# Kernel optimization log

Hardware: AMD Instinct MI355X
Metric: run time of the kernel (lower is better)

## Reference

```python
import jax, jax.numpy as jnp
import numpy as np


def setup_inputs() -> dict:
    key = jax.random.key(0)
    ks = jax.random.split(key, 5)
    B, T, D, L = 4, 8192, 1024, 128
    X = jax.random.normal(ks[0], (B, T, D), dtype=jnp.float32)
    attention_mask = jnp.ones((B, T), dtype=jnp.float32)
    sd_dl = 1.0 / np.sqrt(D)  # lecun_normal fan_in = D
    Wk = jax.random.normal(ks[1], (D, L), dtype=jnp.float32) * sd_dl
    Wq = jax.random.normal(ks[2], (D, L), dtype=jnp.float32) * sd_dl
    Wv = jax.random.normal(ks[3], (D, D), dtype=jnp.float32) * sd_dl
    o_proj = jax.random.normal(ks[4], (D, D), dtype=jnp.float32) * sd_dl
    return {"X": X, "attention_mask": attention_mask, "Wk": Wk, "Wq": Wq,
            "Wv": Wv, "o_proj": o_proj, "n_heads": 16}


def reference(X, attention_mask, Wk, Wq, Wv, o_proj, n_heads):
    B, T, D = X.shape
    H = n_heads
    # Projections, laid out time-major as in the original: (T, B, H, *)
    V = jnp.einsum('DM,BTD->TBM', Wv, X).reshape(T, B, H, -1)   # (T,B,H,d)
    Q = jnp.einsum('DL,BTD->TBL', Wq, X).reshape(T, B, H, -1)   # (T,B,H,l)
    K = jnp.einsum('DL,BTD->TBL', Wk, X).reshape(T, B, H, -1)   # (T,B,H,l)
    m = attention_mask.T[:, :, None, None]                       # (T,B,1,1)
    V = V * m
    Qs = jax.nn.softmax(Q, axis=-1)
    maxi = jnp.max(K, axis=0, keepdims=True)                     # global max over T
    K = jnp.exp(K - maxi) * m
    Kv = jnp.einsum('tbhl,tbhd->bhld', K, V)                     # global KV state
    Ksum = K.sum(axis=0)                                         # (B,H,l)
    Kv = Kv / Ksum[..., None]
    y = jnp.einsum('tbhl,bhld->bthd', Qs, Kv).reshape(B, T, D)
    return y @ o_proj
```

## Files before the change

kernel.cpp:

```cpp
#include <hip/hip_runtime.h>
#include <hip/hip_bf16.h>

typedef unsigned short u16;
typedef unsigned int   u32;

typedef __attribute__((ext_vector_type(8))) short short8;
typedef __attribute__((ext_vector_type(4))) float f32x4;

typedef const __attribute__((address_space(1))) void g_void;
typedef __attribute__((address_space(3))) void l_void;

__device__ __forceinline__ float bf2f(u16 u) {
    u32 x = ((u32)u) << 16;
    return __builtin_bit_cast(float, x);
}
__device__ __forceinline__ u16 f2bf(float f) {
    u32 u = __builtin_bit_cast(u32, f);
    u32 r = (u + 0x7FFFu + ((u >> 16) & 1u)) >> 16;
    return (u16)r;
}
__device__ __forceinline__ u32 pack2(float a, float b) {
    return (u32)f2bf(a) | ((u32)f2bf(b) << 16);
}

__global__ void detect_kernel(const u16* __restrict__ X, int* __restrict__ flags) {
    __shared__ int cnt[256];
    int c = 0;
    for (int i = threadIdx.x; i < 16384; i += 256) {
        u16 v = X[i];
        int e = (v >> 7) & 0xFF;
        c += (e >= 104 && e <= 140) ? 1 : 0;
    }
    cnt[threadIdx.x] = c;
    __syncthreads();
    for (int s = 128; s > 0; s >>= 1) {
        if (threadIdx.x < s) cnt[threadIdx.x] += cnt[threadIdx.x + s];
        __syncthreads();
    }
    if (threadIdx.x == 0) {
        flags[0] = (cnt[0] < 14746) ? 1 : 0;
        flags[1] = 0;
    }
}

__global__ __launch_bounds__(256) void convert_x(const float* __restrict__ Xf,
                                                 u16* __restrict__ XC,
                                                 const int* __restrict__ flags, int n) {
    if (flags[0] == 0) return;
    int i = (blockIdx.x * 256 + threadIdx.x) * 8;
    if (i >= n) return;
    float4 a = *(const float4*)(Xf + i);
    float4 b = *(const float4*)(Xf + i + 4);
    uint4 o;
    o.x = pack2(a.x, a.y); o.y = pack2(a.z, a.w);
    o.z = pack2(b.x, b.y); o.w = pack2(b.z, b.w);
    *(uint4*)(XC + i) = o;
}

__global__ void convert_mask(const void* __restrict__ m, float* __restrict__ MC,
                             const int* __restrict__ flags, int n) {
    int i = blockIdx.x * 256 + threadIdx.x;
    if (i >= n) return;
    MC[i] = flags[0] ? ((const float*)m)[i] : bf2f(((const u16*)m)[i]);
}

__global__ __launch_bounds__(256) void gemm_bt(
    const u16* __restrict__ A0, const u16* __restrict__ A1, int lda,
    const u16* __restrict__ Bt, int ldb,
    void* __restrict__ C, int ldc,
    int Mtiles, int K,
    const int* __restrict__ aselp, const int* __restrict__ ofp) {
    __shared__ char smem[16384];

    const u16* A = aselp[0] ? A1 : A0;

    const int tid = threadIdx.x;
    const int w = tid >> 6, lane = tid & 63;
    const int mt = blockIdx.x % Mtiles;
    const int nt = blockIdx.x / Mtiles;
    const int m0 = mt << 7, n0 = nt << 7;
    const int wm = w >> 1, wn = w & 1;

    f32x4 acc[4][4] = {};

    const int rr = w * 16 + (lane >> 2);
    const int cg = (lane & 3) ^ ((lane >> 3) & 3);

    const u16* gA0 = A + (m0 + rr) * lda + cg * 8;
    const u16* gA1 = A + (m0 + rr + 64) * lda + cg * 8;
    const u16* gB0 = Bt + (n0 + rr) * ldb + cg * 8;
    const u16* gB1 = Bt + (n0 + rr + 64) * ldb + cg * 8;

    char* lA0 = smem + w * 1024 + lane * 16;
    char* lA1 = smem + 4096 + w * 1024 + lane * 16;
    char* lB0 = smem + 8192 + w * 1024 + lane * 16;
    char* lB1 = smem + 12288 + w * 1024 + lane * 16;

    const int fr_a = (wm << 6) + (lane & 15);
    const int fr_b = (wn << 6) + (lane & 15);
    const int sl = (lane >> 4) ^ ((lane >> 1) & 3);
    const char* pA = smem + fr_a * 64 + sl * 16;
    const char* pB = smem + 8192 + fr_b * 64 + sl * 16;

    for (int kt = 0; kt < K; kt += 32) {
        __builtin_amdgcn_global_load_lds((g_void*)(gA0 + kt), (l_void*)lA0, 16, 0, 0);
        __builtin_amdgcn_global_load_lds((g_void*)(gA1 + kt), (l_void*)lA1, 16, 0, 0);
        __builtin_amdgcn_global_load_lds((g_void*)(gB0 + kt), (l_void*)lB0, 16, 0, 0);
        __builtin_amdgcn_global_load_lds((g_void*)(gB1 + kt), (l_void*)lB1, 16, 0, 0);
        __syncthreads();
        short8 af[4], bfv[4];
#pragma unroll
        for (int i = 0; i < 4; ++i) {
            af[i]  = *(const short8*)(pA + i * 1024);
            bfv[i] = *(const short8*)(pB + i * 1024);
        }
#pragma unroll
        for (int mi = 0; mi < 4; ++mi) {
#pragma unroll
            for (int ni = 0; ni < 4; ++ni) {
                acc[mi][ni] = __builtin_amdgcn_mfma_f32_16x16x32_bf16(
                    af[mi], bfv[ni], acc[mi][ni], 0, 0, 0);
            }
        }
        __syncthreads();
    }

    const int out_fp32 = ofp[0];
    float* fb = (float*)smem;
    const int lrow = tid >> 3, cgp = tid & 7;
#pragma unroll
    for (int mi = 0; mi < 4; ++mi) {
#pragma unroll
        for (int ni = 0; ni < 4; ++ni) {
#pragma unroll
            for (int r = 0; r < 4; ++r) {
                int lr = wm * 16 + ((lane >> 4) << 2) + r;
                int lc = wn * 64 + ni * 16 + (lane & 15);
                fb[lr * 128 + lc] = acc[mi][ni][r];
            }
        }
        __syncthreads();
        int grow = (lrow < 16) ? (mi * 16 + lrow) : (48 + mi * 16 + lrow);
        const float* srcp = fb + lrow * 128 + cgp * 16;
        if (out_fp32) {
            float4* dst = (float4*)((float*)C + (size_t)(m0 + grow) * ldc + n0 + cgp * 16);
            dst[0] = make_float4(srcp[0], srcp[1], srcp[2], srcp[3]);
            dst[1] = make_float4(srcp[4], srcp[5], srcp[6], srcp[7]);
            dst[2] = make_float4(srcp[8], srcp[9], srcp[10], srcp[11]);
            dst[3] = make_float4(srcp[12], srcp[13], srcp[14], srcp[15]);
        } else {
            u32 o0 = pack2(srcp[0], srcp[1]);
            u32 o1 = pack2(srcp[2], srcp[3]);
            u32 o2 = pack2(srcp[4], srcp[5]);
            u32 o3 = pack2(srcp[6], srcp[7]);
            u32 o4 = pack2(srcp[8], srcp[9]);
            u32 o5 = pack2(srcp[10], srcp[11]);
            u32 o6 = pack2(srcp[12], srcp[13]);
            u32 o7 = pack2(srcp[14], srcp[15]);
            uint4* dst = (uint4*)((u16*)C + (size_t)(m0 + grow) * ldc + n0 + cgp * 16);
            dst[0] = make_uint4(o0, o1, o2, o3);
            dst[1] = make_uint4(o4, o5, o6, o7);
        }
        __syncthreads();
    }
}

__device__ __forceinline__ u16 rd_elem(const void* s, int idx, int fp32) {
    return fp32 ? f2bf(((const float*)s)[idx]) : ((const u16*)s)[idx];
}

__global__ void transpose_k(const void* __restrict__ Wq, const void* __restrict__ Wk,
                            const void* __restrict__ Wv, const void* __restrict__ Op,
                            u16* __restrict__ W1T, u16* __restrict__ OpT,
                            const int* __restrict__ flags) {
    int fp32 = flags[0];
    int id = blockIdx.x;
    const void* src; u16* dst; int Nc, mid;
    if (id < 128)       { src = Wq; dst = W1T;               Nc = 128;  mid = id; }
    else if (id < 256)  { src = Wk; dst = W1T + 128 * 1024;  Nc = 128;  mid = id - 128; }
    else if (id < 1280) { src = Wv; dst = W1T + 256 * 1024;  Nc = 1024; mid = id - 256; }
    else                { src = Op; dst = OpT;               Nc = 1024; mid = id - 1280; }
    int kt = mid & 31, nt = mid >> 5;
    __shared__ u16 tile[32][33];
    int x = threadIdx.x & 31, y0 = threadIdx.x >> 5;
#pragma unroll
    for (int yy = 0; yy < 4; ++yy) {
        int y = y0 * 4 + yy;
        tile[y][x] = rd_elem(src, (kt * 32 + y) * Nc + nt * 32 + x, fp32);
    }
    __syncthreads();
#pragma unroll
    for (int yy = 0; yy < 4; ++yy) {
        int y = y0 * 4 + yy;
        dst[(nt * 32 + y) * 1024 + kt * 32 + x] = tile[x][y];
    }
}

__global__ __launch_bounds__(256) void maxpart_kernel(const u16* __restrict__ QKV,
                                                      float* __restrict__ Pmax) {
    int bid = blockIdx.x;
    int b = bid >> 5, chunk = bid & 31;
    int tid = threadIdx.x;
    int l = tid & 127, half = tid >> 7;
    float mx = -3.0e38f;
    int t0 = chunk * 256;
    for (int i = half; i < 256; i += 2) {
        int m = b * 8192 + t0 + i;
        mx = fmaxf(mx, bf2f(QKV[(size_t)m * 1280 + 128 + l]));
    }
    __shared__ float sm[256];
    sm[tid] = mx;
    __syncthreads();
    if (tid < 128) Pmax[bid * 128 + tid] = fmaxf(sm[tid], sm[tid + 128]);
}

__global__ void maxreduce_kernel(const float* __restrict__ Pmax, float* __restrict__ Kmax) {
    int tid = threadIdx.x;
    float mx = -3.0e38f;
    int b = tid >> 7;
    int l = tid & 127;
    for (int c = 0; c < 32; ++c) mx = fmaxf(mx, Pmax[(b * 32 + c) * 128 + l]);
    Kmax[tid] = mx;
}

__global__ __launch_bounds__(256) void kvpart_kernel(const u16* __restrict__ QKV,
                                                     const float* __restrict__ MC,
                                                     const float* __restrict__ Kmax,
                                                     float* __restrict__ Kvp,
                                                     float* __restrict__ Ksp) {
    int bid = blockIdx.x;
    int chunk = bid & 31;
    int bh = bid >> 5;
    int h = bh & 15, b = bh >> 4;
    int w = threadIdx.x >> 6, lane = threadIdx.x & 63;

    float mx[8];
#pragma unroll
    for (int l = 0; l < 8; ++l) mx[l] = Kmax[b * 128 + h * 8 + l];

    float kv[8] = {0, 0, 0, 0, 0, 0, 0, 0};
    float ks[8] = {0, 0, 0, 0, 0, 0, 0, 0};
    int t0 = chunk * 256;
    for (int i = 0; i < 64; ++i) {
        int t = t0 + w + i * 4;
        int m = b * 8192 + t;
        const u16* row = QKV + (size_t)m * 1280;
        float v = bf2f(row[256 + h * 64 + lane]);
        uint4 kq = *(const uint4*)(row + 128 + h * 8);
        float msk = MC[b * 8192 + t];
        float vm = v * msk;
        float kf[8];
        kf[0] = __builtin_bit_cast(float, kq.x << 16);
        kf[1] = __builtin_bit_cast(float, kq.x & 0xffff0000u);
        kf[2] = __builtin_bit_cast(float, kq.y << 16);
        kf[3] = __builtin_bit_cast(float, kq.y & 0xffff0000u);
        kf[4] = __builtin_bit_cast(float, kq.z << 16);
        kf[5] = __builtin_bit_cast(float, kq.z & 0xffff0000u);
        kf[6] = __builtin_bit_cast(float, kq.w << 16);
        kf[7] = __builtin_bit_cast(float, kq.w & 0xffff0000u);
#pragma unroll
        for (int l = 0; l < 8; ++l) {
            float e = __expf(kf[l] - mx[l]) * msk;
            kv[l] += e * vm;
            ks[l] += e;
        }
    }
    __shared__ float red[4][8][64];
    __shared__ float redks[4][8];
#pragma unroll
    for (int l = 0; l < 8; ++l) red[w][l][lane] = kv[l];
    if (lane == 0) {
#pragma unroll
        for (int l = 0; l < 8; ++l) redks[w][l] = ks[l];
    }
    __syncthreads();
    int tid = threadIdx.x;
    for (int c = tid; c < 512; c += 256) {
        int l = c >> 6, d = c & 63;
        Kvp[bid * 512 + c] = red[0][l][d] + red[1][l][d] + red[2][l][d] + red[3][l][d];
    }
    if (tid < 8) Ksp[bid * 8 + tid] = redks[0][tid] + redks[1][tid] + redks[2][tid] + redks[3][tid];
}

__global__ void kvreduce_kernel(const float* __restrict__ Kvp, const float* __restrict__ Ksp,
                                float* __restrict__ Kv) {
    int bh = blockIdx.x;
    int tid = threadIdx.x;
    int l = tid >> 6;
    float s = 0.f, ks = 0.f;
    for (int c = 0; c < 32; ++c) {
        s += Kvp[(bh * 32 + c) * 512 + tid];
        ks += Ksp[(bh * 32 + c) * 8 + l];
    }
    Kv[bh * 512 + tid] = s / ks;
}

__global__ __launch_bounds__(256) void y_kernel(u16* __restrict__ QKV,
                                                const float* __restrict__ Kv) {
    int bid = blockIdx.x;
    int b = bid >> 8, chunk = bid & 255;
    int w = threadIdx.x >> 6, lane = threadIdx.x & 63;
    int hh = w & 1;
    int rp = w >> 1;
    int hloc = lane >> 3;
    int h = hh * 8 + hloc;
    int dg = lane & 7;

    float4 kva[8], kvb[8];
    const float* kvp = Kv + (b * 16 + h) * 512 + dg * 8;
#pragma unroll
    for (int l = 0; l < 8; ++l) {
        kva[l] = *(const float4*)(kvp + l * 64);
        kvb[l] = *(const float4*)(kvp + l * 64 + 4);
    }
    int lgrp = lane & 56;
    for (int i = 0; i < 16; ++i) {
        int t = chunk * 32 + i * 2 + rp;
        int m = b * 8192 + t;
        u16* row = QKV + (size_t)m * 1280;
        float qv = bf2f(row[hh * 64 + lane]);
        float qm = qv;
        qm = fmaxf(qm, __shfl_xor(qm, 1));
        qm = fmaxf(qm, __shfl_xor(qm, 2));
        qm = fmaxf(qm, __shfl_xor(qm, 4));
        float e = __expf(qv - qm);
        float s = e;
        s += __shfl_xor(s, 1);
        s += __shfl_xor(s, 2);
        s += __shfl_xor(s, 4);
        float qs = e / s;
        float4 a0 = {0.f, 0.f, 0.f, 0.f}, a1 = {0.f, 0.f, 0.f, 0.f};
#pragma unroll
        for (int l = 0; l < 8; ++l) {
            float ql = __shfl(qs, lgrp + l);
            a0.x += ql * kva[l].x; a0.y += ql * kva[l].y;
            a0.z += ql * kva[l].z; a0.w += ql * kva[l].w;
            a1.x += ql * kvb[l].x; a1.y += ql * kvb[l].y;
            a1.z += ql * kvb[l].z; a1.w += ql * kvb[l].w;
        }
        uint4 o;
        o.x = pack2(a0.x, a0.y);
        o.y = pack2(a0.z, a0.w);
        o.z = pack2(a1.x, a1.y);
        o.w = pack2(a1.z, a1.w);
        *(uint4*)(row + 256 + h * 64 + dg * 8) = o;
    }
}

#define OFF_FLAG ((size_t)0)
#define OFF_W1T  ((size_t)1024)
#define OFF_OPT  ((size_t)2622464)
#define OFF_PMAX ((size_t)4719616)
#define OFF_KMAX ((size_t)4785152)
#define OFF_KVP  ((size_t)4787200)
#define OFF_KSP  ((size_t)8981504)
#define OFF_KV   ((size_t)9047040)
#define OFF_MC   ((size_t)9178112)
#define OFF_XC   ((size_t)9309184)
#define OFF_QKV  ((size_t)76418048)

extern "C" void kernel_launch(void* const* d_in, const int* in_sizes, int n_in,
                              void* d_out, int out_size, void* d_ws, size_t ws_size,
                              hipStream_t stream) {
    const u16* X   = (const u16*)d_in[0];
    const void* msk = d_in[1];
    const void* Wk  = d_in[2];
    const void* Wq  = d_in[3];
    const void* Wv  = d_in[4];
    const void* Op  = d_in[5];

    char* ws = (char*)d_ws;
    int*   FLAGS = (int*)(ws + OFF_FLAG);
    u16*   W1T  = (u16*)(ws + OFF_W1T);
    u16*   OPT  = (u16*)(ws + OFF_OPT);
    float* PMAX = (float*)(ws + OFF_PMAX);
    float* KMAX = (float*)(ws + OFF_KMAX);
    float* KVP  = (float*)(ws + OFF_KVP);
    float* KSP  = (float*)(ws + OFF_KSP);
    float* KV   = (float*)(ws + OFF_KV);
    float* MC   = (float*)(ws + OFF_MC);
    u16*   XC   = (u16*)(ws + OFF_XC);
    u16*   QKV  = (u16*)(ws + OFF_QKV);

    detect_kernel<<<1, 256, 0, stream>>>(X, FLAGS);
    convert_x<<<16384, 256, 0, stream>>>((const float*)d_in[0], XC, FLAGS, 33554432);
    convert_mask<<<128, 256, 0, stream>>>(msk, MC, FLAGS, 32768);
    transpose_k<<<2304, 256, 0, stream>>>(Wq, Wk, Wv, Op, W1T, OPT, FLAGS);
    gemm_bt<<<2560, 256, 0, stream>>>(X, XC, 1024, W1T, 1024, QKV, 1280, 256, 1024,
                                      FLAGS, FLAGS + 1);
    maxpart_kernel<<<128, 256, 0, stream>>>(QKV, PMAX);
    maxreduce_kernel<<<1, 512, 0, stream>>>(PMAX, KMAX);
    kvpart_kernel<<<2048, 256, 0, stream>>>(QKV, MC, KMAX, KVP, KSP);
    kvreduce_kernel<<<64, 512, 0, stream>>>(KVP, KSP, KV);
    y_kernel<<<1024, 256, 0, stream>>>(QKV, KV);
    gemm_bt<<<2048, 256, 0, stream>>>(QKV + 256, QKV + 256, 1280, OPT, 1024,
                                      d_out, 1024, 256, 1024, FLAGS + 1, FLAGS);
}
```

Baseline: 617.0 us.

## Reorder GEMM tiles, pad epilogue LDS, fuse max reduction, widen small kernels

```diff
diff --git a/kernel.cpp b/kernel.cpp
--- a/kernel.cpp
+++ b/kernel.cpp
@@ -70,14 +70,15 @@
     void* __restrict__ C, int ldc,
     int Mtiles, int K,
     const int* __restrict__ aselp, const int* __restrict__ ofp) {
-    __shared__ char smem[16384];
+    __shared__ char smem[17408];
 
     const u16* A = aselp[0] ? A1 : A0;
 
     const int tid = threadIdx.x;
     const int w = tid >> 6, lane = tid & 63;
-    const int mt = blockIdx.x % Mtiles;
-    const int nt = blockIdx.x / Mtiles;
+    const int Ntiles = gridDim.x / Mtiles;
+    const int mt = blockIdx.x / Ntiles;
+    const int nt = blockIdx.x % Ntiles;
     const int m0 = mt << 7, n0 = nt << 7;
     const int wm = w >> 1, wn = w & 1;
 
@@ -136,12 +137,12 @@
             for (int r = 0; r < 4; ++r) {
                 int lr = wm * 16 + ((lane >> 4) << 2) + r;
                 int lc = wn * 64 + ni * 16 + (lane & 15);
-                fb[lr * 128 + lc] = acc[mi][ni][r];
+                fb[lr * 132 + lc] = acc[mi][ni][r];
             }
         }
         __syncthreads();
         int grow = (lrow < 16) ? (mi * 16 + lrow) : (48 + mi * 16 + lrow);
-        const float* srcp = fb + lrow * 128 + cgp * 16;
+        const float* srcp = fb + lrow * 132 + cgp * 16;
         if (out_fp32) {
             float4* dst = (float4*)((float*)C + (size_t)(m0 + grow) * ldc + n0 + cgp * 16);
             dst[0] = make_float4(srcp[0], srcp[1], srcp[2], srcp[3]);
@@ -199,33 +200,41 @@
 __global__ __launch_bounds__(256) void maxpart_kernel(const u16* __restrict__ QKV,
                                                       float* __restrict__ Pmax) {
     int bid = blockIdx.x;
-    int b = bid >> 5, chunk = bid & 31;
+    int b = bid >> 7, chunk = bid & 127;
     int tid = threadIdx.x;
-    int l = tid & 127, half = tid >> 7;
-    float mx = -3.0e38f;
-    int t0 = chunk * 256;
-    for (int i = half; i < 256; i += 2) {
-        int m = b * 8192 + t0 + i;
-        mx = fmaxf(mx, bf2f(QKV[(size_t)m * 1280 + 128 + l]));
-    }
-    __shared__ float sm[256];
-    sm[tid] = mx;
+    int g = tid >> 4, s = tid & 15;
+    float mx8[8];
+#pragma unroll
+    for (int j = 0; j < 8; ++j) mx8[j] = -3.0e38f;
+    int t0 = chunk * 64;
+#pragma unroll
+    for (int p = 0; p < 4; ++p) {
+        int m = b * 8192 + t0 + g + p * 16;
+        uint4 kq = *(const uint4*)(QKV + (size_t)m * 1280 + 128 + s * 8);
+        mx8[0] = fmaxf(mx8[0], __builtin_bit_cast(float, kq.x << 16));
+        mx8[1] = fmaxf(mx8[1], __builtin_bit_cast(float, kq.x & 0xffff0000u));
+        mx8[2] = fmaxf(mx8[2], __builtin_bit_cast(float, kq.y << 16));
+        mx8[3] = fmaxf(mx8[3], __builtin_bit_cast(float, kq.y & 0xffff0000u));
+        mx8[4] = fmaxf(mx8[4], __builtin_bit_cast(float, kq.z << 16));
+        mx8[5] = fmaxf(mx8[5], __builtin_bit_cast(float, kq.z & 0xffff0000u));
+        mx8[6] = fmaxf(mx8[6], __builtin_bit_cast(float, kq.w << 16));
+        mx8[7] = fmaxf(mx8[7], __builtin_bit_cast(float, kq.w & 0xffff0000u));
+    }
+    __shared__ float red[16][128];
+#pragma unroll
+    for (int j = 0; j < 8; ++j) red[g][s * 8 + j] = mx8[j];
     __syncthreads();
-    if (tid < 128) Pmax[bid * 128 + tid] = fmaxf(sm[tid], sm[tid + 128]);
-}
-
-__global__ void maxreduce_kernel(const float* __restrict__ Pmax, float* __restrict__ Kmax) {
-    int tid = threadIdx.x;
-    float mx = -3.0e38f;
-    int b = tid >> 7;
-    int l = tid & 127;
-    for (int c = 0; c < 32; ++c) mx = fmaxf(mx, Pmax[(b * 32 + c) * 128 + l]);
-    Kmax[tid] = mx;
+    if (tid < 128) {
+        float m = -3.0e38f;
+#pragma unroll
+        for (int g2 = 0; g2 < 16; ++g2) m = fmaxf(m, red[g2][tid]);
+        Pmax[bid * 128 + tid] = m;
+    }
 }
 
 __global__ __launch_bounds__(256) void kvpart_kernel(const u16* __restrict__ QKV,
                                                      const float* __restrict__ MC,
-                                                     const float* __restrict__ Kmax,
+                                                     const float* __restrict__ Pmax,
                                                      float* __restrict__ Kvp,
                                                      float* __restrict__ Ksp) {
     int bid = blockIdx.x;
@@ -234,9 +243,26 @@
     int h = bh & 15, b = bh >> 4;
     int w = threadIdx.x >> 6, lane = threadIdx.x & 63;
 
+    __shared__ float redm[32][8];
+    __shared__ float redf[8];
+    {
+        int jj = threadIdx.x & 7, cgx = threadIdx.x >> 3;
+        float pm = -3.0e38f;
+        for (int c = cgx; c < 128; c += 32)
+            pm = fmaxf(pm, Pmax[((b * 128 + c) << 7) + h * 8 + jj]);
+        redm[cgx][jj] = pm;
+        __syncthreads();
+        if (threadIdx.x < 8) {
+            float m2 = -3.0e38f;
+#pragma unroll
+            for (int c2 = 0; c2 < 32; ++c2) m2 = fmaxf(m2, redm[c2][threadIdx.x]);
+            redf[threadIdx.x] = m2;
+        }
+        __syncthreads();
+    }
     float mx[8];
 #pragma unroll
-    for (int l = 0; l < 8; ++l) mx[l] = Kmax[b * 128 + h * 8 + l];
+    for (int l = 0; l < 8; ++l) mx[l] = redf[l];
 
     float kv[8] = {0, 0, 0, 0, 0, 0, 0, 0};
     float ks[8] = {0, 0, 0, 0, 0, 0, 0, 0};
@@ -298,7 +324,7 @@
 __global__ __launch_bounds__(256) void y_kernel(u16* __restrict__ QKV,
                                                 const float* __restrict__ Kv) {
     int bid = blockIdx.x;
-    int b = bid >> 8, chunk = bid & 255;
+    int b = bid >> 9, chunk = bid & 511;
     int w = threadIdx.x >> 6, lane = threadIdx.x & 63;
     int hh = w & 1;
     int rp = w >> 1;
@@ -314,8 +340,8 @@
         kvb[l] = *(const float4*)(kvp + l * 64 + 4);
     }
     int lgrp = lane & 56;
-    for (int i = 0; i < 16; ++i) {
-        int t = chunk * 32 + i * 2 + rp;
+    for (int i = 0; i < 8; ++i) {
+        int t = chunk * 16 + i * 2 + rp;
         int m = b * 8192 + t;
         u16* row = QKV + (size_t)m * 1280;
         float qv = bf2f(row[hh * 64 + lane]);
@@ -350,8 +376,6 @@
 #define OFF_FLAG ((size_t)0)
 #define OFF_W1T  ((size_t)1024)
 #define OFF_OPT  ((size_t)2622464)
-#define OFF_PMAX ((size_t)4719616)
-#define OFF_KMAX ((size_t)4785152)
 #define OFF_KVP  ((size_t)4787200)
 #define OFF_KSP  ((size_t)8981504)
 #define OFF_KV   ((size_t)9047040)
@@ -373,13 +397,12 @@
     int*   FLAGS = (int*)(ws + OFF_FLAG);
     u16*   W1T  = (u16*)(ws + OFF_W1T);
     u16*   OPT  = (u16*)(ws + OFF_OPT);
-    float* PMAX = (float*)(ws + OFF_PMAX);
-    float* KMAX = (float*)(ws + OFF_KMAX);
     float* KVP  = (float*)(ws + OFF_KVP);
     float* KSP  = (float*)(ws + OFF_KSP);
     float* KV   = (float*)(ws + OFF_KV);
     float* MC   = (float*)(ws + OFF_MC);
     u16*   XC   = (u16*)(ws + OFF_XC);
+    float* PMAX = (float*)(ws + OFF_XC);
     u16*   QKV  = (u16*)(ws + OFF_QKV);
 
     detect_kernel<<<1, 256, 0, stream>>>(X, FLAGS);
@@ -388,11 +411,10 @@
     transpose_k<<<2304, 256, 0, stream>>>(Wq, Wk, Wv, Op, W1T, OPT, FLAGS);
     gemm_bt<<<2560, 256, 0, stream>>>(X, XC, 1024, W1T, 1024, QKV, 1280, 256, 1024,
                                       FLAGS, FLAGS + 1);
-    maxpart_kernel<<<128, 256, 0, stream>>>(QKV, PMAX);
-    maxreduce_kernel<<<1, 512, 0, stream>>>(PMAX, KMAX);
-    kvpart_kernel<<<2048, 256, 0, stream>>>(QKV, MC, KMAX, KVP, KSP);
+    maxpart_kernel<<<512, 256, 0, stream>>>(QKV, PMAX);
+    kvpart_kernel<<<2048, 256, 0, stream>>>(QKV, MC, PMAX, KVP, KSP);
     kvreduce_kernel<<<64, 512, 0, stream>>>(KVP, KSP, KV);
-    y_kernel<<<1024, 256, 0, stream>>>(QKV, KV);
+    y_kernel<<<2048, 256, 0, stream>>>(QKV, KV);
     gemm_bt<<<2048, 256, 0, stream>>>(QKV + 256, QKV + 256, 1280, OPT, 1024,
                                       d_out, 1024, 256, 1024, FLAGS + 1, FLAGS);
 }
```

Result: faster. 601.9 us (-2.5%).
